# Kernel tuning notes

Hardware: AMD Instinct MI355X
Metric: run time of the kernel (lower is better)

Reference implementation:

```python
import jax, jax.numpy as jnp
import numpy as np

B, T_TREES, LEAVES = 1024, 34, 16
E = 128            # entity = logic = theorem embedding size
N_NF, N_LF = 4, 3  # binary numerical / logic function experts
V_ENT, V_TH = 2000, 32
GT_MAX, ENT_MAX, TH_MAX = 8, 16, 8


def setup_inputs() -> dict:
    key = jax.random.key(0)
    ks = jax.random.split(key, 24)
    s2e = 1.0 / np.sqrt(2 * E)
    s4e = 1.0 / np.sqrt(4 * E)
    se = 1.0 / np.sqrt(E)
    inp = {
        'leaf_idx': jax.random.randint(ks[0], (B, T_TREES, LEAVES), 0, V_ENT),
        'nf_ids':   jax.random.randint(ks[1], (B, T_TREES, 15), 0, N_NF),
        'lf_ids':   jax.random.randint(ks[2], (B, GT_MAX + 1), 0, N_LF),
        'th_idx':   jax.random.randint(ks[3], (B, TH_MAX), 0, V_TH),
        'ent_emb':  jax.random.normal(ks[4], (V_ENT, E)) * 0.02,
        'th_emb':   jax.random.normal(ks[5], (V_TH, E)) * 0.02,
        # nf two2one expert MLPs: Linear(2E,2E) -> ReLU -> Linear(2E,E)
        'nf_W1': jax.random.normal(ks[6], (N_NF, 2 * E, 2 * E)) * s2e,
        'nf_b1': jnp.zeros((N_NF, 2 * E)),
        'nf_W2': jax.random.normal(ks[7], (N_NF, 2 * E, E)) * s2e,
        'nf_b2': jnp.zeros((N_NF, E)),
        # lf two2one expert MLPs: Linear(2E,4E) -> ReLU -> Linear(4E,E)
        'lf_W1': jax.random.normal(ks[8], (N_LF, 2 * E, 4 * E)) * s2e,
        'lf_b1': jnp.zeros((N_LF, 4 * E)),
        'lf_W2': jax.random.normal(ks[9], (N_LF, 4 * E, E)) * s4e,
        'lf_b2': jnp.zeros((N_LF, E)),
        # higher attention linears: logic_size -> {entity,entity,theorem} size
        'he_W': jax.random.normal(ks[10], (E, E)) * se, 'he_b': jnp.zeros((E,)),
        'hg_W': jax.random.normal(ks[11], (E, E)) * se, 'hg_b': jnp.zeros((E,)),
        'ht_W': jax.random.normal(ks[12], (E, E)) * se, 'ht_b': jnp.zeros((E,)),
    }
    return inp


def _expert_mlp(x, ids, W1, b1, W2, b2):
    # x: [..., Din], ids: [...] selecting among K experts; masked sum over K (small fixed loop)
    out = jnp.zeros(x.shape[:-1] + (W2.shape[-1],), x.dtype)
    for k in range(W1.shape[0]):
        h = jax.nn.relu(x @ W1[k] + b1[k]) @ W2[k] + b2[k]
        out = out + jnp.where((ids == k)[..., None], h, 0.0)
    return out


def _attend(keys, q):
    # keys: [B, N, D], q: [B, D] -> attentive context [B, D]
    a = jax.nn.softmax(jnp.einsum('bnd,bd->bn', keys, q), axis=-1)
    return jnp.einsum('bn,bnd->bd', a, keys)


def _forward(leaf_idx, nf_ids, lf_ids, th_idx, ent_emb, th_emb,
             nf_W1, nf_b1, nf_W2, nf_b2, lf_W1, lf_b1, lf_W2, lf_b2,
             he_W, he_b, hg_W, hg_b, ht_W, ht_b):
    # leaf entity embedding lookup: [B, 34, 16, E]
    cur = ent_emb[leaf_idx]
    # recursive tree reduction over 4 levels of binary nf MLPs (batched over all nodes)
    off = 0
    for lvl in range(4):
        n = LEAVES >> (lvl + 1)  # nodes at this level: 8,4,2,1
        x = cur.reshape(cur.shape[0], T_TREES, n, 2 * E)  # concat(left,right)
        ids = nf_ids[..., off:off + n]
        off += n
        cur = _expert_mlp(x, ids, nf_W1, nf_b1, nf_W2, nf_b2)
    roots = cur[..., 0, :]                       # [B, 34, E]
    ent = roots[:, :ENT_MAX]                     # [B, 16, E] standalone entities
    pairs = roots[:, ENT_MAX:].reshape(roots.shape[0], GT_MAX + 1, 2 * E)
    stmt = _expert_mlp(pairs, lf_ids, lf_W1, lf_b1, lf_W2, lf_b2)  # [B, 9, E]
    gt = stmt[:, :GT_MAX]                        # [B, 8, E] ground truths
    obj = stmt[:, GT_MAX]                        # [B, E]    objective
    th = th_emb[th_idx]                          # [B, 8, E] theorems
    ent_ctx = _attend(ent, obj @ he_W + he_b)
    gt_ctx = _attend(gt, obj @ hg_W + hg_b)
    th_ctx = _attend(th, obj @ ht_W + ht_b)
    # higher attentive state: 2*L + E + T = 512
    return jnp.concatenate([obj, gt_ctx, ent_ctx, th_ctx], axis=-1)


def reference(leaf_idx, nf_ids, lf_ids, th_idx, ent_emb, th_emb,
              nf_W1, nf_b1, nf_W2, nf_b2, lf_W1, lf_b1, lf_W2, lf_b2,
              he_W, he_b, hg_W, hg_b, ht_W, ht_b):
    return _forward(leaf_idx, nf_ids, lf_ids, th_idx, ent_emb, th_emb,
                    nf_W1, nf_b1, nf_W2, nf_b2, lf_W1, lf_b1, lf_W2, lf_b2,
                    he_W, he_b, hg_W, hg_b, ht_W, ht_b)
```

## Files before the change

kernel.cpp:

```cpp
#include <hip/hip_runtime.h>
#include <math.h>


typedef unsigned short u16;
typedef unsigned int   u32;
typedef unsigned long long u64;
typedef __attribute__((ext_vector_type(8))) short v8s;
typedef __attribute__((ext_vector_type(4))) float f32x4;

__device__ __forceinline__ float b2f(u16 u) { return __uint_as_float(((u32)u) << 16); }
__device__ __forceinline__ u16 f2b(float f) {
  f = (f == f) ? f : 0.f;
  u32 x = __float_as_uint(f);
  u32 r = x + 0x7fffu + ((x >> 16) & 1u);
  return (u16)(r >> 16);
}

#define NTREE 34816
#define RLEAF 9216


__global__ __launch_bounds__(256) void perm_hist_k(
    const int* __restrict__ nf, int* __restrict__ bh,
    const int CB, const int bt0, const int nb)
{
  const int gid = blockIdx.x * 256 + threadIdx.x;
  int id = -1, lr = 0, cofs = 12, ioff = 14, shift = 0;
  if (gid < 8 * CB)       { lr = gid;          cofs = 0;  ioff = 0;  shift = 3; }
  else if (gid < 12 * CB) { lr = gid - 8*CB;   cofs = 4;  ioff = 8;  shift = 2; }
  else if (gid < 14 * CB) { lr = gid - 12*CB;  cofs = 8;  ioff = 12; shift = 1; }
  else if (gid < 15 * CB) { lr = gid - 14*CB;          }
  if (gid < 15 * CB) {
    int bt = bt0 + (lr >> shift);
    int n  = lr & ((1 << shift) - 1);
    id = nf[bt * 15 + ioff + n];
  }
  __shared__ int lcnt[16];
  if (threadIdx.x < 16) lcnt[threadIdx.x] = 0;
  __syncthreads();
  const int lane = threadIdx.x & 63;
  #pragma unroll
  for (int e = 0; e < 4; ++e) {
    u64 m = __ballot(id == e);
    if (m && lane == __builtin_ctzll(m))
      atomicAdd(&lcnt[cofs + e], (int)__popcll(m));
  }
  __syncthreads();
  if (threadIdx.x < 16)
    bh[threadIdx.x * nb + blockIdx.x] = lcnt[threadIdx.x];
}

__global__ __launch_bounds__(1024) void perm_scan_k(
    int* __restrict__ bh, int* __restrict__ cnt, const int nb)
{
  const int s = threadIdx.x >> 6;
  const int lane = threadIdx.x & 63;
  int carry = 0;
  for (int b0 = 0; b0 < nb; b0 += 64) {
    const int b = b0 + lane;
    int v = (b < nb) ? bh[s * nb + b] : 0;
    int x = v;
    #pragma unroll
    for (int d = 1; d < 64; d <<= 1) {
      int y = __shfl_up(x, d);
      if (lane >= d) x += y;
    }
    if (b < nb) bh[s * nb + b] = carry + x - v;
    carry += __shfl(x, 63);
  }
  if (lane == 0) cnt[s] = carry;
}

__global__ __launch_bounds__(256) void perm_scatter_k(
    const int* __restrict__ nf, const int* __restrict__ bh,
    int* __restrict__ perm, const int CB, const int bt0, const int nb)
{
  const int gid = blockIdx.x * 256 + threadIdx.x;
  int id = -1, lr = 0, rows = CB, cofs = 12, pofs = 56 * CB, ioff = 14, shift = 0;
  if (gid < 8 * CB)       { lr = gid;          rows = 8*CB; cofs = 0;  pofs = 0;      ioff = 0;  shift = 3; }
  else if (gid < 12 * CB) { lr = gid - 8*CB;   rows = 4*CB; cofs = 4;  pofs = 32*CB;  ioff = 8;  shift = 2; }
  else if (gid < 14 * CB) { lr = gid - 12*CB;  rows = 2*CB; cofs = 8;  pofs = 48*CB;  ioff = 12; shift = 1; }
  else if (gid < 15 * CB) { lr = gid - 14*CB;                 }
  if (gid < 15 * CB) {
    int bt = bt0 + (lr >> shift);
    int n  = lr & ((1 << shift) - 1);
    id = nf[bt * 15 + ioff + n];
  }
  __shared__ int wc[4][16];
  const int w = threadIdx.x >> 6, lane = threadIdx.x & 63;
  if (lane < 16) wc[w][lane] = 0;
  __syncthreads();
  u64 msave[4];
  #pragma unroll
  for (int e = 0; e < 4; ++e) {
    u64 m = __ballot(id == e);
    msave[e] = m;
    if (m && lane == __builtin_ctzll(m))
      wc[w][cofs + e] = (int)__popcll(m);
  }
  __syncthreads();
  #pragma unroll
  for (int e = 0; e < 4; ++e) {
    if (id == e) {
      const int slot = cofs + e;
      int base = bh[slot * nb + blockIdx.x];
      #pragma unroll
      for (int w2 = 0; w2 < 3; ++w2)
        if (w2 < w) base += wc[w2][slot];
      perm[pofs + e * rows + base +
           (int)__popcll(msave[e] & ((1ull << lane) - 1ull))] = lr;
    }
  }
}

__global__ __launch_bounds__(256) void leaf_perm_k(
    const int* __restrict__ lf, int* __restrict__ cnt, int* __restrict__ perm)
{
  const int gid = blockIdx.x * 256 + threadIdx.x;
  const int id = lf[gid];
  const int lane = threadIdx.x & 63;
  for (int e = 0; e < 3; ++e) {
    u64 m = __ballot(id == e);
    if (!m) continue;
    int leader = __builtin_ctzll(m);
    int bp = 0;
    if (lane == leader) bp = atomicAdd(&cnt[e], (int)__popcll(m));
    bp = __shfl(bp, leader);
    if (id == e)
      perm[e * RLEAF + bp + (int)__popcll(m & ((1ull << lane) - 1ull))] = gid;
  }
}

__global__ __launch_bounds__(256) void transpose_k(
    const float* __restrict__ s0, const float* __restrict__ s1,
    const float* __restrict__ s2, const float* __restrict__ s3,
    const float* __restrict__ s4,
    u16* __restrict__ d0, u16* __restrict__ d1, u16* __restrict__ d2,
    u16* __restrict__ d3, u16* __restrict__ d4)
{
  __shared__ float tile[16][17];
  const int t = threadIdx.x;
  const int idx0 = blockIdx.x * 256;
  if (idx0 < 983040) {
    const float* s; u16* d; int tb, estr, O, kt, mt, e;
    int tloc0;
    if (idx0 < 262144)      { s = s0; d = d0; tb = 0;      estr = 65536;  O = 256; }
    else if (idx0 < 393216) { s = s1; d = d1; tb = 262144; estr = 32768;  O = 128; }
    else if (idx0 < 786432) { s = s2; d = d2; tb = 393216; estr = 131072; O = 512; }
    else                    { s = s3; d = d3; tb = 786432; estr = 65536;  O = 128; }
    tloc0 = idx0 - tb;
    const int blk = tloc0 >> 9;
    const int hb  = (tloc0 >> 8) & 1;
    if (idx0 < 262144)      { kt = blk & 7;  mt = (blk >> 3) & 15; e = blk >> 7; }
    else if (idx0 < 393216) { kt = blk & 7;  mt = (blk >> 3) & 7;  e = blk >> 6; }
    else if (idx0 < 786432) { kt = blk & 7;  mt = (blk >> 3) & 31; e = blk >> 8; }
    else                    { kt = blk & 15; mt = (blk >> 4) & 7;  e = blk >> 7; }
    const int o0 = mt * 16;
    const int k0 = kt * 32 + hb * 16;
    tile[t >> 4][t & 15] = s[(size_t)e * estr + (size_t)(k0 + (t >> 4)) * O + o0 + (t & 15)];
    __syncthreads();
    d[tloc0 + t] = f2b(tile[((t >> 7) << 3) + (t & 7)][(t >> 3) & 15]);
  } else {
    int tl = idx0 + t - 983040;
    d4[tl] = f2b(s4[tl]);
  }
}

template<int HID, int NEXP, int MODE, int MR>
__global__ __launch_bounds__(256, 2) void mlp_k(
    const u16* __restrict__ src, const int* __restrict__ lidx,
    const u16* __restrict__ emb,
    const int* __restrict__ perm, const int* __restrict__ cnt,
    const int rows, const int bt0,
    const u16* __restrict__ W1f, const float* __restrict__ b1,
    const u16* __restrict__ W2f, const float* __restrict__ b2,
    u16* __restrict__ dst)
{
  constexpr int NT  = MR / 16;
  constexpr int MT1 = HID / 64;
  constexpr int K2  = HID / 32;
  constexpr bool PREF1 = (MT1 <= 4);
  constexpr int XB  = MR * 512;
  constexpr int HB  = MR * HID * 2;
  constexpr int UB  = XB > HB ? XB : HB;
  __shared__ __align__(16) char uni[UB];
  __shared__ int prc[MR], rid[MR], soff[2 * MR];
  u16* const xs = (u16*)uni;
  u16* const hs = (u16*)uni;

  int bin = -1, tile = 0, cb = 0;
  {
    int rem = blockIdx.x;
    #pragma unroll
    for (int e = 0; e < NEXP; ++e) {
      int ce = cnt[e];
      int tt = (ce + MR - 1) / MR;
      if (bin < 0) {
        if (rem < tt) { bin = e; tile = rem; cb = ce; }
        else rem -= tt;
      }
    }
  }
  if (bin < 0) return;
  const int rbase = tile * MR;
  const int tid = threadIdx.x;
  const int w  = tid >> 6;
  const int lane = tid & 63;
  const int lm = lane & 15;
  const int lq = lane >> 4;

  const u16* const W1b = W1f + ((size_t)(bin * (HID / 16) + w * MT1) << 12) + lane * 8;
  const u16* const W2b = W2f + ((size_t)((bin * 8 + w * 2) * K2) << 9) + lane * 8;

  v8s afb[3][PREF1 ? MT1 : 1];
  if (PREF1) {
    #pragma unroll
    for (int m = 0; m < MT1; ++m)
      afb[0][m] = *(const v8s*)(W1b + (size_t)(m * 8) * 512);
    #pragma unroll
    for (int m = 0; m < MT1; ++m)
      afb[1][m] = *(const v8s*)(W1b + (size_t)(m * 8 + 1) * 512);
  }

  if (tid < MR) {
    int rl = rbase + tid;
    int rlc = rl < cb ? rl : (cb - 1);
    rlc = rlc < 0 ? 0 : rlc;
    int rc = perm[(size_t)bin * rows + rlc];
    rc = rc < 0 ? 0 : (rc >= rows ? rows - 1 : rc);
    prc[tid] = rc;
    rid[tid] = (rl < cb) ? rc : -1;
  }
  __syncthreads();

  if (MODE == 0) {
    if (tid < 2 * MR) {
      int r = tid >> 1, h = tid & 1;
      int rc = prc[r];
      int bt = bt0 + (rc >> 3), node = rc & 7;
      int ix = lidx[bt * 16 + node * 2 + h];
      ix = ix < 0 ? 0 : (ix > 1999 ? 1999 : ix);
      soff[tid] = ix * 256;
    }
  } else {
    if (tid < MR) {
      int rc = prc[tid];
      int base;
      if (MODE == 1) base = rc * 512;
      else { int bq = rc / 9, g = rc - bq * 9; base = (bq * 34 + 16 + 2 * g) * 256; }
      soff[2 * tid]     = base;
      soff[2 * tid + 1] = base + 256;
    }
  }
  __syncthreads();

  const char* const sb = (MODE == 0) ? (const char*)emb : (const char*)src;
  #pragma unroll
  for (int i = 0; i < MR / 8; ++i) {
    int c = i * 256 + tid;
    int seg = c >> 4, sub = c & 15;
    uint4 v = *(const uint4*)(sb + (size_t)(u32)soff[seg] + sub * 16);
    int r = seg >> 1;
    int c32 = ((seg & 1) << 4) + sub;
    int cs = c32 ^ ((r & 7) << 1);
    *(uint4*)(uni + r * 512 + cs * 16) = v;
  }
  __syncthreads();

  f32x4 acc[MT1][NT];
  #pragma unroll
  for (int m = 0; m < MT1; ++m)
    #pragma unroll
    for (int n = 0; n < NT; ++n)
      acc[m][n] = f32x4{0.f, 0.f, 0.f, 0.f};

  if (PREF1) {
    #pragma unroll
    for (int k = 0; k < 8; ++k) {
      const int cur = k % 3;
      if (k < 6) {
        const int nx2 = (k + 2) % 3;
        #pragma unroll
        for (int m = 0; m < MT1; ++m)
          afb[nx2][m] = *(const v8s*)(W1b + (size_t)(m * 8 + k + 2) * 512);
      }
      v8s bfr[NT];
      #pragma unroll
      for (int n = 0; n < NT; ++n) {
        int r = n * 16 + lm;
        int cs = (k * 4 + lq) ^ ((lm & 7) << 1);
        bfr[n] = *(const v8s*)(xs + r * 256 + cs * 8);
      }
      #pragma unroll
      for (int m = 0; m < MT1; ++m)
        #pragma unroll
        for (int n = 0; n < NT; ++n)
          acc[m][n] = __builtin_amdgcn_mfma_f32_16x16x32_bf16(afb[cur][m], bfr[n], acc[m][n], 0, 0, 0);
    }
  } else {
    #pragma unroll
    for (int k = 0; k < 8; ++k) {
      v8s bfr[NT];
      #pragma unroll
      for (int n = 0; n < NT; ++n) {
        int r = n * 16 + lm;
        int cs = (k * 4 + lq) ^ ((lm & 7) << 1);
        bfr[n] = *(const v8s*)(xs + r * 256 + cs * 8);
      }
      #pragma unroll
      for (int m = 0; m < MT1; ++m) {
        const v8s af = *(const v8s*)(W1b + (size_t)(m * 8 + k) * 512);
        #pragma unroll
        for (int n = 0; n < NT; ++n)
          acc[m][n] = __builtin_amdgcn_mfma_f32_16x16x32_bf16(af, bfr[n], acc[m][n], 0, 0, 0);
      }
    }
  }

  v8s afb2[3][2];
  #pragma unroll
  for (int m = 0; m < 2; ++m)
    afb2[0][m] = *(const v8s*)(W2b + (size_t)(m * K2) * 512);
  #pragma unroll
  for (int m = 0; m < 2; ++m)
    afb2[1][m] = *(const v8s*)(W2b + (size_t)(m * K2 + 1) * 512);

  __syncthreads();

  const float* b1b = b1 + bin * HID;
  #pragma unroll
  for (int m = 0; m < MT1; ++m) {
    const int f = (w * MT1 + m) * 16 + lq * 4;
    float bb0 = b1b[f], bb1 = b1b[f + 1], bb2 = b1b[f + 2], bb3 = b1b[f + 3];
    #pragma unroll
    for (int n = 0; n < NT; ++n) {
      union { u16 h[4]; uint2 v; } pk;
      f32x4 a = acc[m][n];
      pk.h[0] = f2b(fmaxf(a.x + bb0, 0.f));
      pk.h[1] = f2b(fmaxf(a.y + bb1, 0.f));
      pk.h[2] = f2b(fmaxf(a.z + bb2, 0.f));
      pk.h[3] = f2b(fmaxf(a.w + bb3, 0.f));
      int r = n * 16 + lm;
      int cs = (f >> 3) ^ ((lm & 7) << 1);
      *(uint2*)(uni + (size_t)r * (HID * 2) + (cs << 4) + (f & 7) * 2) = pk.v;
    }
  }
  __syncthreads();

  f32x4 acc2[2][NT];
  #pragma unroll
  for (int m = 0; m < 2; ++m)
    #pragma unroll
    for (int n = 0; n < NT; ++n)
      acc2[m][n] = f32x4{0.f, 0.f, 0.f, 0.f};

  #pragma unroll
  for (int k = 0; k < K2; ++k) {
    const int cur = k % 3;
    if (k < K2 - 2) {
      const int nx2 = (k + 2) % 3;
      #pragma unroll
      for (int m = 0; m < 2; ++m)
        afb2[nx2][m] = *(const v8s*)(W2b + (size_t)(m * K2 + k + 2) * 512);
    }
    v8s bfr[NT];
    #pragma unroll
    for (int n = 0; n < NT; ++n) {
      int r = n * 16 + lm;
      int cs = (k * 4 + lq) ^ ((lm & 7) << 1);
      bfr[n] = *(const v8s*)(hs + (size_t)r * HID + cs * 8);
    }
    #pragma unroll
    for (int m = 0; m < 2; ++m)
      #pragma unroll
      for (int n = 0; n < NT; ++n)
        acc2[m][n] = __builtin_amdgcn_mfma_f32_16x16x32_bf16(afb2[cur][m], bfr[n], acc2[m][n], 0, 0, 0);
  }

  __syncthreads();
  const float* b2b = b2 + bin * 128;
  #pragma unroll
  for (int m = 0; m < 2; ++m) {
    const int f = (w * 2 + m) * 16 + lq * 4;
    float bb0 = b2b[f], bb1 = b2b[f + 1], bb2 = b2b[f + 2], bb3 = b2b[f + 3];
    #pragma unroll
    for (int n = 0; n < NT; ++n) {
      union { u16 h[4]; uint2 v; } pk;
      f32x4 a = acc2[m][n];
      pk.h[0] = f2b(a.x + bb0);
      pk.h[1] = f2b(a.y + bb1);
      pk.h[2] = f2b(a.z + bb2);
      pk.h[3] = f2b(a.w + bb3);
      int r = n * 16 + lm;
      int c = (w * 2 + m) * 2 + (lq >> 1);
      int cs = c ^ ((r & 7) << 1);
      *(uint2*)(uni + r * 256 + cs * 16 + (lq & 1) * 8) = pk.v;
    }
  }
  __syncthreads();
  #pragma unroll
  for (int i = 0; i < MR / 16; ++i) {
    int cg = i * 256 + tid;
    int r = cg >> 4, sub = cg & 15;
    int rg = rid[r];
    if (rg >= 0) {
      uint4 v = *(const uint4*)(uni + r * 256 + ((sub ^ ((r & 7) << 1)) << 4));
      *(uint4*)((char*)dst + (size_t)rg * 256 + sub * 16) = v;
    }
  }
}

__global__ __launch_bounds__(128) void attn_k(
    const u16* __restrict__ stmt, const u16* __restrict__ roots,
    const float* __restrict__ themb, const int* __restrict__ thidx,
    const float* __restrict__ wHe, const float* __restrict__ bHe,
    const float* __restrict__ wHg, const float* __restrict__ bHg,
    const float* __restrict__ wHt, const float* __restrict__ bHt,
    float* __restrict__ out)
{
  const int b = blockIdx.x, t = threadIdx.x;
  __shared__ float obj_s[128], q_s[128], keys_s[16 * 132], a_s[16];

  const float obj = b2f(stmt[((size_t)b * 9 + 8) * 128 + t]);
  obj_s[t] = obj;
  out[(size_t)b * 512 + t] = obj;
  __syncthreads();

  for (int a = 0; a < 3; ++a) {
    int cntk;
    const float *Wt, *bv;
    if (a == 0) {
      cntk = 8; Wt = wHg; bv = bHg;
      for (int j = 0; j < 8; ++j)
        keys_s[j * 132 + t] = b2f(stmt[((size_t)b * 9 + j) * 128 + t]);
    } else if (a == 1) {
      cntk = 16; Wt = wHe; bv = bHe;
      for (int j = 0; j < 16; ++j)
        keys_s[j * 132 + t] = b2f(roots[((size_t)b * 34 + j) * 128 + t]);
    } else {
      cntk = 8; Wt = wHt; bv = bHt;
      for (int j = 0; j < 8; ++j) {
        int ti = thidx[b * 8 + j] & 31;
        keys_s[j * 132 + t] = themb[(size_t)ti * 128 + t];
      }
    }
    float qa = bv[t];
    for (int k = 0; k < 128; ++k) qa += obj_s[k] * Wt[k * 128 + t];
    q_s[t] = (qa == qa) ? qa : 0.f;
    __syncthreads();
    {
      int j = t >> 3, s = t & 7;
      if (j < cntk) {
        float sc = 0.f;
        #pragma unroll
        for (int k = 0; k < 16; ++k)
          sc += keys_s[j * 132 + s * 16 + k] * q_s[s * 16 + k];
        sc += __shfl_xor(sc, 1);
        sc += __shfl_xor(sc, 2);
        sc += __shfl_xor(sc, 4);
        if (s == 0) a_s[j] = (sc == sc) ? sc : 0.f;
      }
    }
    __syncthreads();
    if (t < 16) {
      float v = (t < cntk) ? a_s[t] : -3.0e38f;
      float mx = v;
      #pragma unroll
      for (int d = 1; d < 16; d <<= 1) mx = fmaxf(mx, __shfl_xor(mx, d));
      float e = (t < cntk) ? expf(v - mx) : 0.f;
      float sm = e;
      #pragma unroll
      for (int d = 1; d < 16; d <<= 1) sm += __shfl_xor(sm, d);
      if (t < cntk) a_s[t] = e / sm;
    }
    __syncthreads();
    float c = 0.f;
    for (int j = 0; j < cntk; ++j) c += a_s[j] * keys_s[j * 132 + t];
    out[(size_t)b * 512 + 128 * (a + 1) + t] = c;
    __syncthreads();
  }
}

extern "C" void kernel_launch(void* const* d_in, const int* in_sizes, int n_in,
                              void* d_out, int out_size, void* d_ws, size_t ws_size,
                              hipStream_t stream)
{
  const int*   leaf_idx = (const int*)d_in[0];
  const int*   nf_ids   = (const int*)d_in[1];
  const int*   lf_ids   = (const int*)d_in[2];
  const int*   th_idx   = (const int*)d_in[3];
  const float* ent_emb  = (const float*)d_in[4];
  const float* th_emb   = (const float*)d_in[5];
  const float* nf_W1 = (const float*)d_in[6];
  const float* nf_b1 = (const float*)d_in[7];
  const float* nf_W2 = (const float*)d_in[8];
  const float* nf_b2 = (const float*)d_in[9];
  const float* lf_W1 = (const float*)d_in[10];
  const float* lf_b1 = (const float*)d_in[11];
  const float* lf_W2 = (const float*)d_in[12];
  const float* lf_b2 = (const float*)d_in[13];
  const float* he_W = (const float*)d_in[14];
  const float* he_b = (const float*)d_in[15];
  const float* hg_W = (const float*)d_in[16];
  const float* hg_b = (const float*)d_in[17];
  const float* ht_W = (const float*)d_in[18];
  const float* ht_b = (const float*)d_in[19];

  int CB = NTREE;
  while (CB > 544 && 14500000ull + (unsigned long long)CB * 3320ull > (unsigned long long)ws_size)
    CB >>= 1;
  const int nch = NTREE / CB;
  const int NB = (15 * CB + 255) / 256;

  char* ws = (char*)d_ws;
  size_t off = 0;
  auto take = [&](size_t bytes) -> char* {
    char* p = ws + off;
    off = (off + bytes + 255) & ~(size_t)255;
    return p;
  };
  int* cnt      = (int*)take(8192);
  int* leafperm = (int*)take((size_t)3 * RLEAF * 4);
  int* chperm   = (int*)take((size_t)60 * CB * 4);
  int* bh       = (int*)take((size_t)16 * NB * 4);
  u16* wN1  = (u16*)take((size_t)4 * 256 * 256 * 2);
  u16* wN2  = (u16*)take((size_t)4 * 128 * 256 * 2);
  u16* wL1  = (u16*)take((size_t)3 * 512 * 256 * 2);
  u16* wL2  = (u16*)take((size_t)3 * 128 * 512 * 2);
  u16* embB = (u16*)take((size_t)2000 * 128 * 2);
  u16* bufA  = (u16*)take((size_t)CB * 8 * 128 * 2);
  u16* bufB  = (u16*)take((size_t)CB * 4 * 128 * 2);
  u16* roots = (u16*)take((size_t)NTREE * 128 * 2);
  u16* stmt  = (u16*)take((size_t)RLEAF * 128 * 2);

  int* leafcnt = cnt + nch * 16;

  hipMemsetAsync(cnt, 0, (size_t)(nch * 16 + 8) * 4, stream);
  transpose_k<<<4840, 256, 0, stream>>>(nf_W1, nf_W2, lf_W1, lf_W2, ent_emb,
                                        wN1, wN2, wL1, wL2, embB);
  leaf_perm_k<<<36, 256, 0, stream>>>(lf_ids, leafcnt, leafperm);

  for (int c = 0; c < nch; ++c) {
    const int bt0 = c * CB;
    int* ccnt = cnt + c * 16;
    perm_hist_k<<<NB, 256, 0, stream>>>(nf_ids, bh, CB, bt0, NB);
    perm_scan_k<<<1, 1024, 0, stream>>>(bh, ccnt, NB);
    perm_scatter_k<<<NB, 256, 0, stream>>>(nf_ids, bh, chperm, CB, bt0, NB);
    mlp_k<256, 4, 0, 96><<<(8 * CB + 95) / 96 + 4, 256, 0, stream>>>(
        nullptr, leaf_idx, embB, chperm, ccnt, 8 * CB, bt0,
        wN1, nf_b1, wN2, nf_b2, bufA);
    mlp_k<256, 4, 1, 96><<<(4 * CB + 95) / 96 + 4, 256, 0, stream>>>(
        bufA, nullptr, nullptr, chperm + 32 * CB, ccnt + 4, 4 * CB, 0,
        wN1, nf_b1, wN2, nf_b2, bufB);
    mlp_k<256, 4, 1, 96><<<(2 * CB + 95) / 96 + 4, 256, 0, stream>>>(
        bufB, nullptr, nullptr, chperm + 48 * CB, ccnt + 8, 2 * CB, 0,
        wN1, nf_b1, wN2, nf_b2, bufA);
    mlp_k<256, 4, 1, 96><<<(CB + 95) / 96 + 4, 256, 0, stream>>>(
        bufA, nullptr, nullptr, chperm + 56 * CB, ccnt + 12, CB, 0,
        wN1, nf_b1, wN2, nf_b2, roots + (size_t)bt0 * 128);
  }

  mlp_k<512, 3, 2, 32><<<RLEAF / 32 + 3, 256, 0, stream>>>(
      roots, nullptr, nullptr, leafperm, leafcnt, RLEAF, 0,
      wL1, lf_b1, wL2, lf_b2, stmt);

  attn_k<<<1024, 128, 0, stream>>>(stmt, roots, th_emb, th_idx,
                                   he_W, he_b, hg_W, hg_b, ht_W, ht_b,
                                   (float*)d_out);
}
```

Before: 322.8 us.

## Double-buffer LDS operand reads and raise MFMA priority in expert MLP kernel

Both GEMM loops in the expert MLP kernel now prefetch the next k-step's shared-memory B fragments into a second register buffer while the current MFMAs run, and wrap the MFMA block in s_setprio to favour matrix issue. The W1 prefetch is generalised so the large-hidden path also prefetches weights one step ahead. Row-index setup is merged into a single thread phase, removing one barrier and the prc shared array, and row ids are cached in registers. The extra double buffers raise register pressure and could lower occupancy at launch bound 2.

```diff
diff --git a/kernel.cpp b/kernel.cpp
--- a/kernel.cpp
+++ b/kernel.cpp
@@ -179,12 +179,13 @@
   constexpr int NT  = MR / 16;
   constexpr int MT1 = HID / 64;
   constexpr int K2  = HID / 32;
-  constexpr bool PREF1 = (MT1 <= 4);
+  constexpr int PD1 = (MT1 <= 4) ? 2 : 1;
+  constexpr int NB1 = PD1 + 1;
   constexpr int XB  = MR * 512;
   constexpr int HB  = MR * HID * 2;
   constexpr int UB  = XB > HB ? XB : HB;
   __shared__ __align__(16) char uni[UB];
-  __shared__ int prc[MR], rid[MR], soff[2 * MR];
+  __shared__ int rid[MR], soff[2 * MR];
   u16* const xs = (u16*)uni;
   u16* const hs = (u16*)uni;
 
@@ -212,15 +213,12 @@
   const u16* const W1b = W1f + ((size_t)(bin * (HID / 16) + w * MT1) << 12) + lane * 8;
   const u16* const W2b = W2f + ((size_t)((bin * 8 + w * 2) * K2) << 9) + lane * 8;
 
-  v8s afb[3][PREF1 ? MT1 : 1];
-  if (PREF1) {
+  v8s afb[NB1][MT1];
+  #pragma unroll
+  for (int d = 0; d < PD1; ++d)
     #pragma unroll
     for (int m = 0; m < MT1; ++m)
-      afb[0][m] = *(const v8s*)(W1b + (size_t)(m * 8) * 512);
-    #pragma unroll
-    for (int m = 0; m < MT1; ++m)
-      afb[1][m] = *(const v8s*)(W1b + (size_t)(m * 8 + 1) * 512);
-  }
+      afb[d][m] = *(const v8s*)(W1b + (size_t)(m * 8 + d) * 512);
 
   if (tid < MR) {
     int rl = rbase + tid;
@@ -228,23 +226,16 @@
     rlc = rlc < 0 ? 0 : rlc;
     int rc = perm[(size_t)bin * rows + rlc];
     rc = rc < 0 ? 0 : (rc >= rows ? rows - 1 : rc);
-    prc[tid] = rc;
     rid[tid] = (rl < cb) ? rc : -1;
-  }
-  __syncthreads();
-
-  if (MODE == 0) {
-    if (tid < 2 * MR) {
-      int r = tid >> 1, h = tid & 1;
-      int rc = prc[r];
+    if (MODE == 0) {
       int bt = bt0 + (rc >> 3), node = rc & 7;
-      int ix = lidx[bt * 16 + node * 2 + h];
-      ix = ix < 0 ? 0 : (ix > 1999 ? 1999 : ix);
-      soff[tid] = ix * 256;
-    }
-  } else {
-    if (tid < MR) {
-      int rc = prc[tid];
+      int ia = lidx[bt * 16 + node * 2];
+      int ib = lidx[bt * 16 + node * 2 + 1];
+      ia = ia < 0 ? 0 : (ia > 1999 ? 1999 : ia);
+      ib = ib < 0 ? 0 : (ib > 1999 ? 1999 : ib);
+      soff[2 * tid]     = ia * 256;
+      soff[2 * tid + 1] = ib * 256;
+    } else {
       int base;
       if (MODE == 1) base = rc * 512;
       else { int bq = rc / 9, g = rc - bq * 9; base = (bq * 34 + 16 + 2 * g) * 256; }
@@ -267,6 +258,10 @@
   }
   __syncthreads();
 
+  int rdn[NT];
+  #pragma unroll
+  for (int n = 0; n < NT; ++n) rdn[n] = rid[n * 16 + lm];
+
   f32x4 acc[MT1][NT];
   #pragma unroll
   for (int m = 0; m < MT1; ++m)
@@ -274,47 +269,38 @@
     for (int n = 0; n < NT; ++n)
       acc[m][n] = f32x4{0.f, 0.f, 0.f, 0.f};
 
-  if (PREF1) {
-    #pragma unroll
-    for (int k = 0; k < 8; ++k) {
-      const int cur = k % 3;
-      if (k < 6) {
-        const int nx2 = (k + 2) % 3;
-        #pragma unroll
-        for (int m = 0; m < MT1; ++m)
-          afb[nx2][m] = *(const v8s*)(W1b + (size_t)(m * 8 + k + 2) * 512);
-      }
-      v8s bfr[NT];
+  v8s bfr2[2][NT];
+  #pragma unroll
+  for (int n = 0; n < NT; ++n) {
+    int r = n * 16 + lm;
+    int cs = (0 * 4 + lq) ^ ((lm & 7) << 1);
+    bfr2[0][n] = *(const v8s*)(xs + r * 256 + cs * 8);
+  }
+  #pragma unroll
+  for (int k = 0; k < 8; ++k) {
+    const int cur = k % NB1;
+    if (k + PD1 < 8) {
+      const int nx = (k + PD1) % NB1;
+      #pragma unroll
+      for (int m = 0; m < MT1; ++m)
+        afb[nx][m] = *(const v8s*)(W1b + (size_t)(m * 8 + k + PD1) * 512);
+    }
+    const int cb_ = k & 1;
+    if (k < 7) {
       #pragma unroll
       for (int n = 0; n < NT; ++n) {
         int r = n * 16 + lm;
-        int cs = (k * 4 + lq) ^ ((lm & 7) << 1);
-        bfr[n] = *(const v8s*)(xs + r * 256 + cs * 8);
+        int cs = ((k + 1) * 4 + lq) ^ ((lm & 7) << 1);
+        bfr2[cb_ ^ 1][n] = *(const v8s*)(xs + r * 256 + cs * 8);
       }
-      #pragma unroll
-      for (int m = 0; m < MT1; ++m)
-        #pragma unroll
-        for (int n = 0; n < NT; ++n)
-          acc[m][n] = __builtin_amdgcn_mfma_f32_16x16x32_bf16(afb[cur][m], bfr[n], acc[m][n], 0, 0, 0);
-    }
-  } else {
-    #pragma unroll
-    for (int k = 0; k < 8; ++k) {
-      v8s bfr[NT];
-      #pragma unroll
-      for (int n = 0; n < NT; ++n) {
-        int r = n * 16 + lm;
-        int cs = (k * 4 + lq) ^ ((lm & 7) << 1);
-        bfr[n] = *(const v8s*)(xs + r * 256 + cs * 8);
-      }
-      #pragma unroll
-      for (int m = 0; m < MT1; ++m) {
-        const v8s af = *(const v8s*)(W1b + (size_t)(m * 8 + k) * 512);
-        #pragma unroll
-        for (int n = 0; n < NT; ++n)
-          acc[m][n] = __builtin_amdgcn_mfma_f32_16x16x32_bf16(af, bfr[n], acc[m][n], 0, 0, 0);
-      }
-    }
+    }
+    __builtin_amdgcn_s_setprio(1);
+    #pragma unroll
+    for (int m = 0; m < MT1; ++m)
+      #pragma unroll
+      for (int n = 0; n < NT; ++n)
+        acc[m][n] = __builtin_amdgcn_mfma_f32_16x16x32_bf16(afb[cur][m], bfr2[cb_][n], acc[m][n], 0, 0, 0);
+    __builtin_amdgcn_s_setprio(0);
   }
 
   v8s afb2[3][2];
@@ -355,6 +341,12 @@
       acc2[m][n] = f32x4{0.f, 0.f, 0.f, 0.f};
 
   #pragma unroll
+  for (int n = 0; n < NT; ++n) {
+    int r = n * 16 + lm;
+    int cs = (0 * 4 + lq) ^ ((lm & 7) << 1);
+    bfr2[0][n] = *(const v8s*)(hs + (size_t)r * HID + cs * 8);
+  }
+  #pragma unroll
   for (int k = 0; k < K2; ++k) {
     const int cur = k % 3;
     if (k < K2 - 2) {
@@ -363,18 +355,22 @@
       for (int m = 0; m < 2; ++m)
         afb2[nx2][m] = *(const v8s*)(W2b + (size_t)(m * K2 + k + 2) * 512);
     }
-    v8s bfr[NT];
-    #pragma unroll
-    for (int n = 0; n < NT; ++n) {
-      int r = n * 16 + lm;
-      int cs = (k * 4 + lq) ^ ((lm & 7) << 1);
-      bfr[n] = *(const v8s*)(hs + (size_t)r * HID + cs * 8);
-    }
+    const int cb_ = k & 1;
+    if (k < K2 - 1) {
+      #pragma unroll
+      for (int n = 0; n < NT; ++n) {
+        int r = n * 16 + lm;
+        int cs = ((k + 1) * 4 + lq) ^ ((lm & 7) << 1);
+        bfr2[cb_ ^ 1][n] = *(const v8s*)(hs + (size_t)r * HID + cs * 8);
+      }
+    }
+    __builtin_amdgcn_s_setprio(1);
     #pragma unroll
     for (int m = 0; m < 2; ++m)
       #pragma unroll
       for (int n = 0; n < NT; ++n)
-        acc2[m][n] = __builtin_amdgcn_mfma_f32_16x16x32_bf16(afb2[cur][m], bfr[n], acc2[m][n], 0, 0, 0);
+        acc2[m][n] = __builtin_amdgcn_mfma_f32_16x16x32_bf16(afb2[cur][m], bfr2[cb_][n], acc2[m][n], 0, 0, 0);
+    __builtin_amdgcn_s_setprio(0);
   }
 
   __syncthreads();
```

Measured after the change: 300.3 us. 7.0% less time.
